# Kernel optimization log

Hardware: AMD Instinct MI355X
Metric: run time of the kernel (lower is better)

The kernel has to match this reference:

```python
import jax, jax.numpy as jnp
import numpy as np

B, L, H, HKV, D, HID, FFN = 32, 4096, 32, 2, 128, 4096, 13696
ROT = 64  # rotary_dim = kv_channels // 2 (GLM style)
EPS = 1e-5


def setup_inputs() -> dict:
    key = jax.random.key(0)
    ks = jax.random.split(key, 9)
    s = 0.02
    return {
        "hidden_states": jax.random.normal(ks[0], (B, HID), jnp.float32),
        "context_lens": jax.random.randint(ks[1], (B,), 1, L - 1, dtype=jnp.int32),
        "key_cache": jax.random.normal(ks[2], (B, L, HKV, D), jnp.float32),
        "value_cache": jax.random.normal(ks[3], (B, L, HKV, D), jnp.float32),
        "w_ln1": jnp.ones((HID,), jnp.float32),
        "w_ln2": jnp.ones((HID,), jnp.float32),
        "w_qkv": jax.random.normal(ks[4], (HID, H * D + 2 * HKV * D), jnp.float32) * s,
        "b_qkv": jax.random.normal(ks[5], (H * D + 2 * HKV * D,), jnp.float32) * s,
        "w_dense": jax.random.normal(ks[6], (H * D, HID), jnp.float32) * s,
        "w_h4h": jax.random.normal(ks[7], (HID, 2 * FFN), jnp.float32) * s,
        "w_4hh": jax.random.normal(ks[8], (FFN, HID), jnp.float32) * s,
    }


def rmsnorm(x, w):
    v = jnp.mean(x.astype(jnp.float32) ** 2, axis=-1, keepdims=True)
    return (w * (x * jax.lax.rsqrt(v + EPS))).astype(x.dtype)


def apply_rope(x, pos):
    # x: [B, heads, D]; GPT-J interleaved rotary on first ROT dims (glm=True)
    half = ROT // 2
    inv = 1.0 / (10000.0 ** (jnp.arange(half, dtype=jnp.float32) / half))
    f = pos.astype(jnp.float32)[:, None] * inv[None, :]          # [B, half]
    cos, sin = jnp.cos(f)[:, None, :], jnp.sin(f)[:, None, :]    # [B,1,half]
    xr, xp = x[..., :ROT], x[..., ROT:]
    x1, x2 = xr[..., 0::2], xr[..., 1::2]
    rot = jnp.stack([x1 * cos - x2 * sin, x2 * cos + x1 * sin], axis=-1).reshape(xr.shape)
    return jnp.concatenate([rot, xp], axis=-1)


def reference(hidden_states, context_lens, key_cache, value_cache,
              w_ln1, w_ln2, w_qkv, b_qkv, w_dense, w_h4h, w_4hh):
    # input RMSNorm
    ln1 = rmsnorm(hidden_states, w_ln1)
    # fused QKV projection (add_qkv_bias=True)
    qkv = ln1 @ w_qkv + b_qkv
    q, k, v = jnp.split(qkv, [H * D, H * D + HKV * D], axis=-1)
    q = apply_rope(q.reshape(B, H, D), context_lens)
    k = apply_rope(k.reshape(B, HKV, D), context_lens)
    v = v.reshape(B, HKV, D)
    # write new K/V into the paged cache at this token's slot
    kc = key_cache.at[jnp.arange(B), context_lens].set(k)
    vc = value_cache.at[jnp.arange(B), context_lens].set(v)
    # GQA attention: 32 q heads grouped over 2 kv heads
    qg = q.reshape(B, HKV, H // HKV, D)
    scores = jnp.einsum('bghd,blgd->bghl', qg, kc) * (D ** -0.5)
    mask = jnp.arange(L)[None, :] <= context_lens[:, None]       # [B, L]
    scores = jnp.where(mask[:, None, None, :], scores, -jnp.inf)
    p = jax.nn.softmax(scores, axis=-1)
    ctx = jnp.einsum('bghl,blgd->bghd', p, vc).reshape(B, H * D)
    attn_out = ctx @ w_dense                                     # add_bias_linear=False
    x = hidden_states + attn_out                                  # residual pre-LN
    ln2 = rmsnorm(x, w_ln2)
    g, u = jnp.split(ln2 @ w_h4h, 2, axis=-1)
    out = (jax.nn.silu(g) * u) @ w_4hh + x
    return out
```

## Files before the change

### kernel.cpp

```cpp
#include <hip/hip_runtime.h>
#include <hip/hip_bf16.h>

#define B_    32
#define L_    4096
#define H_    32
#define HKV_  2
#define GQ_   16
#define D_    128
#define HID_  4096
#define FFN_  13696
#define NQKV_ 4608
#define ROT_  64
#define EPS_  1e-5f

#define WAVE_POS_ 128
#define NSPLIT_   32

#define KS_QKV_  16
#define KS_DEN_  16
#define KS_H4H_  4
#define KS_4HH_  16

typedef __attribute__((ext_vector_type(8))) __bf16 bf16x8;
typedef __attribute__((ext_vector_type(4))) float  f32x4;

__device__ __forceinline__ void gl_lds16(const float* g, float* l) {
    __builtin_amdgcn_global_load_lds((const __attribute__((address_space(1))) void*)g,
                                     (__attribute__((address_space(3))) void*)l, 16, 0, 0);
}

__global__ __launch_bounds__(1024) void rmsnorm1_k(const float* __restrict__ x,
                                                   const float* __restrict__ w,
                                                   __bf16* __restrict__ out)
{
    int b = blockIdx.x;
    const float* row = x + (size_t)b * HID_;
    float vals[4];
    float ss = 0.f;
#pragma unroll
    for (int i = 0; i < 4; ++i) {
        vals[i] = row[threadIdx.x + i * 1024];
        ss += vals[i] * vals[i];
    }
#pragma unroll
    for (int m = 1; m < 64; m <<= 1) ss += __shfl_xor(ss, m);
    __shared__ float wred[16];
    if ((threadIdx.x & 63) == 0) wred[threadIdx.x >> 6] = ss;
    __syncthreads();
    ss = 0.f;
#pragma unroll
    for (int wv = 0; wv < 16; ++wv) ss += wred[wv];
    float rs = rsqrtf(ss / HID_ + EPS_);
#pragma unroll
    for (int i = 0; i < 4; ++i) {
        int idx = threadIdx.x + i * 1024;
        out[(size_t)b * HID_ + idx] = (__bf16)(w[idx] * vals[i] * rs);
    }
}

template<int K, int N, int KSPLIT>
__global__ __launch_bounds__(256) void gemm16(const __bf16* __restrict__ A,
                                              const float* __restrict__ W,
                                              float* __restrict__ Cp)
{
    static_assert(K % 32 == 0, "K");
    constexpr int ksteps = K / 32;
    const int lane = threadIdx.x & 63;
    const int wid  = threadIdx.x >> 6;
    const int n0   = blockIdx.x * 128;
    const int cw   = wid * 32;
    const int r    = lane & 15;
    const int g4   = lane >> 4;
    const int s0   = (ksteps * (int)blockIdx.y) / KSPLIT;
    const int s1   = (ksteps * (int)(blockIdx.y + 1)) / KSPLIT;

    __shared__ float tiles[3][32][128];

    const int rhalf = lane >> 5;
    const int mslot = lane & 31;
    auto stage = [&](int s, float* dst) {
        if (s >= s1) return;
#pragma unroll
        for (int it = 0; it < 4; ++it) {
            int row  = wid * 8 + it * 2 + rhalf;
            int gcol = ((((mslot >> 1) ^ (row >> 3)) << 3) | ((mslot & 1) << 2));
            const float* src = W + (size_t)(s * 32 + row) * N + n0 + gcol;
            gl_lds16(src, dst + (size_t)(wid * 8 + it * 2) * 128);
        }
    };

    f32x4 acc00 = {0.f,0.f,0.f,0.f}, acc01 = acc00, acc10 = acc00, acc11 = acc00;
    const __bf16* a0p = A + (size_t)r * K;
    const __bf16* a1p = A + (size_t)(r + 16) * K;

    stage(s0,     &tiles[0][0][0]);
    stage(s0 + 1, &tiles[1][0][0]);

    const int c0 = cw + r, c1 = cw + r + 16;
    const int i0 = (((c0 >> 3) ^ g4) << 3) | (c0 & 7);
    const int i1 = (((c1 >> 3) ^ g4) << 3) | (c1 & 7);

    int bufc = 0;
    for (int s = s0; s < s1; ++s) {
        if (s + 1 < s1) asm volatile("s_waitcnt vmcnt(4)" ::: "memory");
        else            asm volatile("s_waitcnt vmcnt(0)" ::: "memory");
        __builtin_amdgcn_s_barrier();
        __builtin_amdgcn_sched_barrier(0);
        int bs = bufc + 2; if (bs >= 3) bs -= 3;
        stage(s + 2, &tiles[bs][0][0]);

        bf16x8 av0 = *(const bf16x8*)(a0p + s * 32 + g4 * 8);
        bf16x8 av1 = *(const bf16x8*)(a1p + s * 32 + g4 * 8);
        const float (*tile)[128] = tiles[bufc];
        bf16x8 b0f, b1f;
#pragma unroll
        for (int j = 0; j < 8; ++j) {
            b0f[j] = (__bf16)tile[g4 * 8 + j][i0];
            b1f[j] = (__bf16)tile[g4 * 8 + j][i1];
        }
        acc00 = __builtin_amdgcn_mfma_f32_16x16x32_bf16(av0, b0f, acc00, 0, 0, 0);
        acc10 = __builtin_amdgcn_mfma_f32_16x16x32_bf16(av1, b0f, acc10, 0, 0, 0);
        acc01 = __builtin_amdgcn_mfma_f32_16x16x32_bf16(av0, b1f, acc01, 0, 0, 0);
        acc11 = __builtin_amdgcn_mfma_f32_16x16x32_bf16(av1, b1f, acc11, 0, 0, 0);
        bufc = (bufc + 1 < 3) ? bufc + 1 : 0;
    }

    float* cp = Cp + ((size_t)blockIdx.y * 32) * N + n0 + cw;
#pragma unroll
    for (int i = 0; i < 4; ++i) {
        cp[(size_t)(g4 * 4 + i) * N + r]           = acc00[i];
        cp[(size_t)(g4 * 4 + i) * N + r + 16]      = acc01[i];
        cp[(size_t)(16 + g4 * 4 + i) * N + r]      = acc10[i];
        cp[(size_t)(16 + g4 * 4 + i) * N + r + 16] = acc11[i];
    }
}

__global__ __launch_bounds__(1024) void qkv_epi_k(const float* __restrict__ part,
                                                  const float* __restrict__ bias,
                                                  const int* __restrict__ ctxl,
                                                  __bf16* __restrict__ qbf,
                                                  float* __restrict__ knew,
                                                  float* __restrict__ vnew)
{
    __shared__ float rowv[NQKV_];
    __shared__ float cs[32], sn[32];
    int b = blockIdx.x;
    int pos = ctxl[b];
    if (threadIdx.x < 32) {
        int t = threadIdx.x;
        float inv = powf(10000.f, -(float)t * (1.0f / 32.0f));
        float f = (float)pos * inv;
        float sv, cv; sincosf(f, &sv, &cv);
        cs[t] = cv; sn[t] = sv;
    }
    for (int i = threadIdx.x; i < NQKV_; i += 1024) {
        float v = bias[i];
#pragma unroll
        for (int p = 0; p < KS_QKV_; ++p) v += part[((size_t)p * B_ + b) * NQKV_ + i];
        rowv[i] = v;
    }
    __syncthreads();
    const float qscale = 0.08838834764831845f;
    for (int i = threadIdx.x; i < HID_; i += 1024) {
        int d = i & 127;
        float o;
        if (d < ROT_) {
            int t = d >> 1;
            float cv = cs[t], sv = sn[t];
            float x1 = rowv[i & ~1], x2 = rowv[i | 1];
            o = (d & 1) ? (x2 * cv + x1 * sv) : (x1 * cv - x2 * sv);
        } else o = rowv[i];
        qbf[(size_t)b * HID_ + i] = (__bf16)(o * qscale);
    }
    if (threadIdx.x < HKV_ * D_) {
        int i = threadIdx.x;
        int d = i & 127;
        float o;
        if (d < ROT_) {
            int t = d >> 1;
            float cv = cs[t], sv = sn[t];
            float x1 = rowv[HID_ + (i & ~1)], x2 = rowv[HID_ + (i | 1)];
            o = (d & 1) ? (x2 * cv + x1 * sv) : (x1 * cv - x2 * sv);
        } else o = rowv[HID_ + i];
        knew[(size_t)b * HKV_ * D_ + i] = o;
        vnew[(size_t)b * HKV_ * D_ + i] = rowv[HID_ + HKV_ * D_ + i];
    }
}

__global__ __launch_bounds__(256) void attn_k(const float* __restrict__ kc,
                                              const float* __restrict__ vc,
                                              const float* __restrict__ knew,
                                              const float* __restrict__ vnew,
                                              const __bf16* __restrict__ qbf,
                                              const int* __restrict__ ctxl,
                                              float* __restrict__ part)
{
    const int bg  = blockIdx.x;
    const int b   = bg >> 1, g = bg & 1;
    const int wid = threadIdx.x >> 6;
    const int split = blockIdx.y * 4 + wid;
    const int ctx = ctxl[b];
    const int p0  = split * WAVE_POS_;
    __shared__ __bf16 plds_all[4][16][40];
    if (p0 > ctx) return;
    const int pend = min(p0 + WAVE_POS_ - 1, ctx);
    const int lane = threadIdx.x & 63;
    const int r = lane & 15, g4 = lane >> 4;

    bf16x8 qf[4];
    {
        const __bf16* qp = qbf + (size_t)b * HID_ + (g * GQ_ + r) * D_ + g4 * 8;
#pragma unroll
        for (int kk = 0; kk < 4; ++kk) qf[kk] = *(const bf16x8*)(qp + kk * 32);
    }
    f32x4 acc[8];
#pragma unroll
    for (int dt = 0; dt < 8; ++dt) acc[dt] = (f32x4){0.f,0.f,0.f,0.f};
    float m_run[4], l_run[4];
#pragma unroll
    for (int i = 0; i < 4; ++i) { m_run[i] = -1e30f; l_run[i] = 0.f; }

    auto plds = plds_all[wid];
    const float* kbase = kc + ((size_t)b * L_ * HKV_ + g) * D_;
    const float* vbase = vc + ((size_t)b * L_ * HKV_ + g) * D_;
    const float* knp = knew + (size_t)(b * HKV_ + g) * D_;
    const float* vnp = vnew + (size_t)(b * HKV_ + g) * D_;

    for (int pc = p0; pc <= pend; pc += 32) {
        f32x4 sf[2];
#pragma unroll
        for (int pt = 0; pt < 2; ++pt) {
            int pos = pc + pt * 16 + r;
            const float* krow = (pos == ctx) ? knp : kbase + (size_t)pos * (HKV_ * D_);
            f32x4 s = {0.f,0.f,0.f,0.f};
#pragma unroll
            for (int kk = 0; kk < 4; ++kk) {
                const float4* kp = (const float4*)(krow + kk * 32 + g4 * 8);
                float4 fa = kp[0], fb = kp[1];
                bf16x8 kf = { (__bf16)fa.x, (__bf16)fa.y, (__bf16)fa.z, (__bf16)fa.w,
                              (__bf16)fb.x, (__bf16)fb.y, (__bf16)fb.z, (__bf16)fb.w };
                s = __builtin_amdgcn_mfma_f32_16x16x32_bf16(qf[kk], kf, s, 0, 0, 0);
            }
            sf[pt] = s;
        }
#pragma unroll
        for (int pt = 0; pt < 2; ++pt) {
            int pos = pc + pt * 16 + r;
            if (pos > ctx) {
#pragma unroll
                for (int i = 0; i < 4; ++i) sf[pt][i] = -1e30f;
            }
        }
#pragma unroll
        for (int i = 0; i < 4; ++i) {
            float mv = fmaxf(sf[0][i], sf[1][i]);
            mv = fmaxf(mv, __shfl_xor(mv, 1));
            mv = fmaxf(mv, __shfl_xor(mv, 2));
            mv = fmaxf(mv, __shfl_xor(mv, 4));
            mv = fmaxf(mv, __shfl_xor(mv, 8));
            float mnew = fmaxf(m_run[i], mv);
            float sc = __expf(m_run[i] - mnew);
            l_run[i] *= sc;
            m_run[i] = mnew;
#pragma unroll
            for (int dt = 0; dt < 8; ++dt) acc[dt][i] *= sc;
        }
#pragma unroll
        for (int pt = 0; pt < 2; ++pt) {
#pragma unroll
            for (int i = 0; i < 4; ++i) {
                float e = __expf(sf[pt][i] - m_run[i]);
                l_run[i] += e;
                plds[g4 * 4 + i][pt * 16 + r] = (__bf16)e;
            }
        }
        asm volatile("s_waitcnt lgkmcnt(0)" ::: "memory");
        __builtin_amdgcn_sched_barrier(0);
        bf16x8 pa = *(const bf16x8*)&plds[r][g4 * 8];
        const float* vrows[8];
#pragma unroll
        for (int j = 0; j < 8; ++j) {
            int pos = pc + g4 * 8 + j;
            vrows[j] = (pos == ctx) ? vnp : vbase + (size_t)pos * (HKV_ * D_);
        }
#pragma unroll
        for (int dt = 0; dt < 8; ++dt) {
            bf16x8 vf;
#pragma unroll
            for (int j = 0; j < 8; ++j) vf[j] = (__bf16)vrows[j][dt * 16 + r];
            acc[dt] = __builtin_amdgcn_mfma_f32_16x16x32_bf16(pa, vf, acc[dt], 0, 0, 0);
        }
        asm volatile("s_waitcnt lgkmcnt(0)" ::: "memory");
        __builtin_amdgcn_sched_barrier(0);
    }
#pragma unroll
    for (int i = 0; i < 4; ++i) {
        float lv = l_run[i];
        lv += __shfl_xor(lv, 1);
        lv += __shfl_xor(lv, 2);
        lv += __shfl_xor(lv, 4);
        lv += __shfl_xor(lv, 8);
        l_run[i] = lv;
    }
    float* pb = part + ((size_t)bg * NSPLIT_ + split) * 16 * 130;
#pragma unroll
    for (int dt = 0; dt < 8; ++dt)
#pragma unroll
        for (int i = 0; i < 4; ++i)
            pb[(g4 * 4 + i) * 130 + dt * 16 + r] = acc[dt][i];
    if (r == 0) {
#pragma unroll
        for (int i = 0; i < 4; ++i) {
            pb[(g4 * 4 + i) * 130 + 128] = m_run[i];
            pb[(g4 * 4 + i) * 130 + 129] = l_run[i];
        }
    }
}

__global__ __launch_bounds__(1024) void attn_comb_k(const float* __restrict__ part,
                                                    const int* __restrict__ ctxl,
                                                    __bf16* __restrict__ ctxb)
{
    int bg = blockIdx.x;
    int c  = blockIdx.y;
    int b = bg >> 1, g = bg & 1;
    int ctx = ctxl[b];
    int ns = ctx / WAVE_POS_ + 1;
    const float* pb = part + (size_t)bg * NSPLIT_ * 16 * 130;
    __shared__ float mlm[NSPLIT_][16], wgt[NSPLIT_][16];
    __shared__ float Mh[16], Ih[16];
    int t = threadIdx.x;
    if (t < NSPLIT_ * 16) {
        int s = t >> 4, h = t & 15;
        mlm[s][h] = pb[(s * 16 + h) * 130 + 128];
        wgt[s][h] = pb[(s * 16 + h) * 130 + 129];
    }
    __syncthreads();
    if (t < 16) {
        int h = t;
        float M = -1e30f;
        for (int s = 0; s < ns; ++s) M = fmaxf(M, mlm[s][h]);
        float den = 0.f;
        for (int s = 0; s < ns; ++s) den += __expf(mlm[s][h] - M) * wgt[s][h];
        Mh[h] = M; Ih[h] = 1.f / den;
    }
    __syncthreads();
    if (t < NSPLIT_ * 16) {
        int s = t >> 4, h = t & 15;
        wgt[s][h] = __expf(mlm[s][h] - Mh[h]) * Ih[h];
    }
    __syncthreads();
    int h = t >> 6, dd = (t & 63) + c * 64;
    float o = 0.f;
    for (int s = 0; s < ns; ++s)
        o += wgt[s][h] * pb[(s * 16 + h) * 130 + dd];
    ctxb[(size_t)b * HID_ + (g * GQ_ + h) * D_ + dd] = (__bf16)o;
}

__global__ __launch_bounds__(1024) void dense_epi_k(const float* __restrict__ hidden,
                                                    const float* __restrict__ partd,
                                                    const float* __restrict__ wln2,
                                                    float* __restrict__ xout,
                                                    __bf16* __restrict__ a2)
{
    __shared__ float xr[HID_];
    int b = blockIdx.x;
    float ss = 0.f;
    for (int i = threadIdx.x; i < HID_; i += 1024) {
        float v = hidden[(size_t)b * HID_ + i];
#pragma unroll
        for (int p = 0; p < KS_DEN_; ++p) v += partd[((size_t)p * B_ + b) * HID_ + i];
        xr[i] = v;
        ss += v * v;
        xout[(size_t)b * HID_ + i] = v;
    }
#pragma unroll
    for (int m = 1; m < 64; m <<= 1) ss += __shfl_xor(ss, m);
    __shared__ float wred[16];
    if ((threadIdx.x & 63) == 0) wred[threadIdx.x >> 6] = ss;
    __syncthreads();
    ss = 0.f;
#pragma unroll
    for (int wv = 0; wv < 16; ++wv) ss += wred[wv];
    float rs = rsqrtf(ss / HID_ + EPS_);
    for (int i = threadIdx.x; i < HID_; i += 1024)
        a2[(size_t)b * HID_ + i] = (__bf16)(wln2[i] * xr[i] * rs);
}

__global__ __launch_bounds__(256) void act_k(const float* __restrict__ gu,
                                             __bf16* __restrict__ act)
{
    int i = blockIdx.x * 256 + threadIdx.x;
    int b = blockIdx.y;
    if (i < FFN_) {
        float gv = 0.f, uv = 0.f;
#pragma unroll
        for (int p = 0; p < KS_H4H_; ++p) {
            const float* gp = gu + ((size_t)p * B_ + b) * 2 * FFN_;
            gv += gp[i];
            uv += gp[FFN_ + i];
        }
        float s = gv / (1.f + __expf(-gv));
        act[(size_t)b * FFN_ + i] = (__bf16)(s * uv);
    }
}

__global__ __launch_bounds__(256) void out_epi_k(const float* __restrict__ x,
                                                 const float* __restrict__ part4,
                                                 float* __restrict__ out)
{
    int i = blockIdx.x * 256 + threadIdx.x;
    float v = x[i];
#pragma unroll
    for (int p = 0; p < KS_4HH_; ++p) v += part4[(size_t)p * (B_ * HID_) + i];
    out[i] = v;
}

extern "C" void kernel_launch(void* const* d_in, const int* in_sizes, int n_in,
                              void* d_out, int out_size, void* d_ws, size_t ws_size,
                              hipStream_t stream)
{
    const float* hidden  = (const float*)d_in[0];
    const int*   ctxl    = (const int*)d_in[1];
    const float* kcache  = (const float*)d_in[2];
    const float* vcache  = (const float*)d_in[3];
    const float* w_ln1   = (const float*)d_in[4];
    const float* w_ln2   = (const float*)d_in[5];
    const float* w_qkv   = (const float*)d_in[6];
    const float* b_qkv   = (const float*)d_in[7];
    const float* w_dense = (const float*)d_in[8];
    const float* w_h4h   = (const float*)d_in[9];
    const float* w_4hh   = (const float*)d_in[10];
    float* out = (float*)d_out;

    char* ws = (char*)d_ws;
    size_t off = 0;
    auto alloc = [&](size_t bytes) -> void* {
        void* p = ws + off;
        off += (bytes + 255) & ~(size_t)255;
        return p;
    };
    __bf16* a0    = (__bf16*)alloc((size_t)B_ * HID_ * 2);
    float*  partq = (float*) alloc((size_t)KS_QKV_ * B_ * NQKV_ * 4);
    __bf16* qbf   = (__bf16*)alloc((size_t)B_ * HID_ * 2);
    float*  knew  = (float*) alloc((size_t)B_ * HKV_ * D_ * 4);
    float*  vnew  = (float*) alloc((size_t)B_ * HKV_ * D_ * 4);
    float*  apart = (float*) alloc((size_t)B_ * HKV_ * NSPLIT_ * 16 * 130 * 4);
    __bf16* ctxb  = (__bf16*)alloc((size_t)B_ * HID_ * 2);
    float*  partd = (float*) alloc((size_t)KS_DEN_ * B_ * HID_ * 4);
    float*  xbuf  = (float*) alloc((size_t)B_ * HID_ * 4);
    __bf16* a2    = (__bf16*)alloc((size_t)B_ * HID_ * 2);
    float*  gu    = (float*) alloc((size_t)KS_H4H_ * B_ * 2 * FFN_ * 4);
    __bf16* actb  = (__bf16*)alloc((size_t)B_ * FFN_ * 2);
    float*  part4 = (float*) alloc((size_t)KS_4HH_ * B_ * HID_ * 4);
    (void)ws_size; (void)in_sizes; (void)n_in; (void)out_size;

    hipLaunchKernelGGL(rmsnorm1_k, dim3(B_), dim3(1024), 0, stream, hidden, w_ln1, a0);
    hipLaunchKernelGGL((gemm16<HID_, NQKV_, KS_QKV_>), dim3(NQKV_ / 128, KS_QKV_), dim3(256), 0, stream, a0, w_qkv, partq);
    hipLaunchKernelGGL(qkv_epi_k, dim3(B_), dim3(1024), 0, stream, partq, b_qkv, ctxl, qbf, knew, vnew);
    hipLaunchKernelGGL(attn_k, dim3(B_ * HKV_, NSPLIT_ / 4), dim3(256), 0, stream,
                       kcache, vcache, knew, vnew, qbf, ctxl, apart);
    hipLaunchKernelGGL(attn_comb_k, dim3(B_ * HKV_, 2), dim3(1024), 0, stream, apart, ctxl, ctxb);
    hipLaunchKernelGGL((gemm16<HID_, HID_, KS_DEN_>), dim3(HID_ / 128, KS_DEN_), dim3(256), 0, stream, ctxb, w_dense, partd);
    hipLaunchKernelGGL(dense_epi_k, dim3(B_), dim3(1024), 0, stream, hidden, partd, w_ln2, xbuf, a2);
    hipLaunchKernelGGL((gemm16<HID_, 2 * FFN_, KS_H4H_>), dim3(2 * FFN_ / 128, KS_H4H_), dim3(256), 0, stream, a2, w_h4h, gu);
    hipLaunchKernelGGL(act_k, dim3((FFN_ + 255) / 256, B_), dim3(256), 0, stream, gu, actb);
    hipLaunchKernelGGL((gemm16<FFN_, HID_, KS_4HH_>), dim3(HID_ / 128, KS_4HH_), dim3(256), 0, stream, actb, w_4hh, part4);
    hipLaunchKernelGGL(out_epi_k, dim3(B_ * HID_ / 256), dim3(256), 0, stream, xbuf, part4, out);
}
```

Baseline: 269.0 us.

## Halve GEMM split-K, double attention splits, and parallelize epilogue kernels across blocks

Lowers the split-K factors of the QKV, dense and 4h-to-h GEMMs from 16 to 8, which shrinks the partial-sum buffers the epilogues must read and reduce. Halves the positions each attention wave handles so twice as many splits run in parallel. The QKV epilogue is spread over four blocks per batch row, and the dense epilogue becomes a grid-parallel reduction plus a separate RMSNorm kernel that combines per-chunk sums of squares. The trade-off is fewer GEMM blocks in flight, more attention partials to combine, and one extra kernel launch.

```diff
diff --git a/kernel.cpp b/kernel.cpp
--- a/kernel.cpp
+++ b/kernel.cpp
@@ -13,13 +13,13 @@
 #define ROT_  64
 #define EPS_  1e-5f
 
-#define WAVE_POS_ 128
-#define NSPLIT_   32
-
-#define KS_QKV_  16
-#define KS_DEN_  16
+#define WAVE_POS_ 64
+#define NSPLIT_   64
+
+#define KS_QKV_  8
+#define KS_DEN_  8
 #define KS_H4H_  4
-#define KS_4HH_  16
+#define KS_4HH_  8
 
 typedef __attribute__((ext_vector_type(8))) __bf16 bf16x8;
 typedef __attribute__((ext_vector_type(4))) float  f32x4;
@@ -142,9 +142,9 @@
                                                   float* __restrict__ knew,
                                                   float* __restrict__ vnew)
 {
-    __shared__ float rowv[NQKV_];
+    __shared__ float rowv[1152];
     __shared__ float cs[32], sn[32];
-    int b = blockIdx.x;
+    int b = blockIdx.x, base = blockIdx.y * 1152;
     int pos = ctxl[b];
     if (threadIdx.x < 32) {
         int t = threadIdx.x;
@@ -153,37 +153,42 @@
         float sv, cv; sincosf(f, &sv, &cv);
         cs[t] = cv; sn[t] = sv;
     }
-    for (int i = threadIdx.x; i < NQKV_; i += 1024) {
+    for (int i0 = threadIdx.x; i0 < 1152; i0 += 1024) {
+        int i = base + i0;
         float v = bias[i];
 #pragma unroll
         for (int p = 0; p < KS_QKV_; ++p) v += part[((size_t)p * B_ + b) * NQKV_ + i];
-        rowv[i] = v;
+        rowv[i0] = v;
     }
     __syncthreads();
     const float qscale = 0.08838834764831845f;
-    for (int i = threadIdx.x; i < HID_; i += 1024) {
+    for (int i0 = threadIdx.x; i0 < 1152; i0 += 1024) {
+        int i = base + i0;
         int d = i & 127;
-        float o;
-        if (d < ROT_) {
-            int t = d >> 1;
-            float cv = cs[t], sv = sn[t];
-            float x1 = rowv[i & ~1], x2 = rowv[i | 1];
-            o = (d & 1) ? (x2 * cv + x1 * sv) : (x1 * cv - x2 * sv);
-        } else o = rowv[i];
-        qbf[(size_t)b * HID_ + i] = (__bf16)(o * qscale);
-    }
-    if (threadIdx.x < HKV_ * D_) {
-        int i = threadIdx.x;
-        int d = i & 127;
-        float o;
-        if (d < ROT_) {
-            int t = d >> 1;
-            float cv = cs[t], sv = sn[t];
-            float x1 = rowv[HID_ + (i & ~1)], x2 = rowv[HID_ + (i | 1)];
-            o = (d & 1) ? (x2 * cv + x1 * sv) : (x1 * cv - x2 * sv);
-        } else o = rowv[HID_ + i];
-        knew[(size_t)b * HKV_ * D_ + i] = o;
-        vnew[(size_t)b * HKV_ * D_ + i] = rowv[HID_ + HKV_ * D_ + i];
+        if (i < HID_) {
+            float o;
+            if (d < ROT_) {
+                int t = d >> 1;
+                float cv = cs[t], sv = sn[t];
+                float x1 = rowv[(i & ~1) - base], x2 = rowv[(i | 1) - base];
+                o = (d & 1) ? (x2 * cv + x1 * sv) : (x1 * cv - x2 * sv);
+            } else o = rowv[i0];
+            qbf[(size_t)b * HID_ + i] = (__bf16)(o * qscale);
+        } else {
+            int j = i - HID_;
+            if (j < HKV_ * D_) {
+                float o;
+                if (d < ROT_) {
+                    int t = d >> 1;
+                    float cv = cs[t], sv = sn[t];
+                    float x1 = rowv[(i & ~1) - base], x2 = rowv[(i | 1) - base];
+                    o = (d & 1) ? (x2 * cv + x1 * sv) : (x1 * cv - x2 * sv);
+                } else o = rowv[i0];
+                knew[(size_t)b * HKV_ * D_ + j] = o;
+            } else {
+                vnew[(size_t)b * HKV_ * D_ + (j - HKV_ * D_)] = rowv[i0];
+            }
+        }
     }
 }
 
@@ -330,7 +335,7 @@
     __shared__ float mlm[NSPLIT_][16], wgt[NSPLIT_][16];
     __shared__ float Mh[16], Ih[16];
     int t = threadIdx.x;
-    if (t < NSPLIT_ * 16) {
+    {
         int s = t >> 4, h = t & 15;
         mlm[s][h] = pb[(s * 16 + h) * 130 + 128];
         wgt[s][h] = pb[(s * 16 + h) * 130 + 129];
@@ -345,7 +350,7 @@
         Mh[h] = M; Ih[h] = 1.f / den;
     }
     __syncthreads();
-    if (t < NSPLIT_ * 16) {
+    {
         int s = t >> 4, h = t & 15;
         wgt[s][h] = __expf(mlm[s][h] - Mh[h]) * Ih[h];
     }
@@ -357,34 +362,44 @@
     ctxb[(size_t)b * HID_ + (g * GQ_ + h) * D_ + dd] = (__bf16)o;
 }
 
-__global__ __launch_bounds__(1024) void dense_epi_k(const float* __restrict__ hidden,
+__global__ __launch_bounds__(1024) void dense_red_k(const float* __restrict__ hidden,
                                                     const float* __restrict__ partd,
-                                                    const float* __restrict__ wln2,
                                                     float* __restrict__ xout,
-                                                    __bf16* __restrict__ a2)
-{
-    __shared__ float xr[HID_];
+                                                    float* __restrict__ ssq)
+{
     int b = blockIdx.x;
-    float ss = 0.f;
-    for (int i = threadIdx.x; i < HID_; i += 1024) {
-        float v = hidden[(size_t)b * HID_ + i];
-#pragma unroll
-        for (int p = 0; p < KS_DEN_; ++p) v += partd[((size_t)p * B_ + b) * HID_ + i];
-        xr[i] = v;
-        ss += v * v;
-        xout[(size_t)b * HID_ + i] = v;
-    }
+    int i = blockIdx.y * 1024 + threadIdx.x;
+    float v = hidden[(size_t)b * HID_ + i];
+#pragma unroll
+    for (int p = 0; p < KS_DEN_; ++p) v += partd[((size_t)p * B_ + b) * HID_ + i];
+    xout[(size_t)b * HID_ + i] = v;
+    float ss = v * v;
 #pragma unroll
     for (int m = 1; m < 64; m <<= 1) ss += __shfl_xor(ss, m);
     __shared__ float wred[16];
     if ((threadIdx.x & 63) == 0) wred[threadIdx.x >> 6] = ss;
     __syncthreads();
-    ss = 0.f;
-#pragma unroll
-    for (int wv = 0; wv < 16; ++wv) ss += wred[wv];
+    if (threadIdx.x == 0) {
+        float s = 0.f;
+#pragma unroll
+        for (int wv = 0; wv < 16; ++wv) s += wred[wv];
+        ssq[b * 4 + blockIdx.y] = s;
+    }
+}
+
+__global__ __launch_bounds__(1024) void rms2_k(const float* __restrict__ xbuf,
+                                               const float* __restrict__ ssq,
+                                               const float* __restrict__ wln2,
+                                               __bf16* __restrict__ a2)
+{
+    int b = blockIdx.x;
+    float ss = ssq[b * 4] + ssq[b * 4 + 1] + ssq[b * 4 + 2] + ssq[b * 4 + 3];
     float rs = rsqrtf(ss / HID_ + EPS_);
-    for (int i = threadIdx.x; i < HID_; i += 1024)
-        a2[(size_t)b * HID_ + i] = (__bf16)(wln2[i] * xr[i] * rs);
+#pragma unroll
+    for (int it = 0; it < 4; ++it) {
+        int i = threadIdx.x + it * 1024;
+        a2[(size_t)b * HID_ + i] = (__bf16)(wln2[i] * xbuf[(size_t)b * HID_ + i] * rs);
+    }
 }
 
 __global__ __launch_bounds__(256) void act_k(const float* __restrict__ gu,
@@ -449,6 +464,7 @@
     __bf16* ctxb  = (__bf16*)alloc((size_t)B_ * HID_ * 2);
     float*  partd = (float*) alloc((size_t)KS_DEN_ * B_ * HID_ * 4);
     float*  xbuf  = (float*) alloc((size_t)B_ * HID_ * 4);
+    float*  ssq   = (float*) alloc((size_t)B_ * 4 * 4);
     __bf16* a2    = (__bf16*)alloc((size_t)B_ * HID_ * 2);
     float*  gu    = (float*) alloc((size_t)KS_H4H_ * B_ * 2 * FFN_ * 4);
     __bf16* actb  = (__bf16*)alloc((size_t)B_ * FFN_ * 2);
@@ -457,12 +473,13 @@
 
     hipLaunchKernelGGL(rmsnorm1_k, dim3(B_), dim3(1024), 0, stream, hidden, w_ln1, a0);
     hipLaunchKernelGGL((gemm16<HID_, NQKV_, KS_QKV_>), dim3(NQKV_ / 128, KS_QKV_), dim3(256), 0, stream, a0, w_qkv, partq);
-    hipLaunchKernelGGL(qkv_epi_k, dim3(B_), dim3(1024), 0, stream, partq, b_qkv, ctxl, qbf, knew, vnew);
+    hipLaunchKernelGGL(qkv_epi_k, dim3(B_, 4), dim3(1024), 0, stream, partq, b_qkv, ctxl, qbf, knew, vnew);
     hipLaunchKernelGGL(attn_k, dim3(B_ * HKV_, NSPLIT_ / 4), dim3(256), 0, stream,
                        kcache, vcache, knew, vnew, qbf, ctxl, apart);
     hipLaunchKernelGGL(attn_comb_k, dim3(B_ * HKV_, 2), dim3(1024), 0, stream, apart, ctxl, ctxb);
     hipLaunchKernelGGL((gemm16<HID_, HID_, KS_DEN_>), dim3(HID_ / 128, KS_DEN_), dim3(256), 0, stream, ctxb, w_dense, partd);
-    hipLaunchKernelGGL(dense_epi_k, dim3(B_), dim3(1024), 0, stream, hidden, partd, w_ln2, xbuf, a2);
+    hipLaunchKernelGGL(dense_red_k, dim3(B_, 4), dim3(1024), 0, stream, hidden, partd, xbuf, ssq);
+    hipLaunchKernelGGL(rms2_k, dim3(B_), dim3(1024), 0, stream, xbuf, ssq, w_ln2, a2);
     hipLaunchKernelGGL((gemm16<HID_, 2 * FFN_, KS_H4H_>), dim3(2 * FFN_ / 128, KS_H4H_), dim3(256), 0, stream, a2, w_h4h, gu);
     hipLaunchKernelGGL(act_k, dim3((FFN_ + 255) / 256, B_), dim3(256), 0, stream, gu, actb);
     hipLaunchKernelGGL((gemm16<FFN_, HID_, KS_4HH_>), dim3(HID_ / 128, KS_4HH_), dim3(256), 0, stream, actb, w_4hh, part4);
```

Result: slower. 297.8 us (+10.7%).
